# Optimization experiments

Hardware: AMD Instinct MI355X
Metric: run time of the kernel (lower is better)

The kernel has to match this reference:

```python
import jax, jax.numpy as jnp
import numpy as np

BATCH, SEQ, HIDDEN = 8, 2048, 1024
WSIZE = 64  # window half-width; eye=True -> positions with |i-j| > WSIZE are masked
NEG_INF = -1e9


def setup_inputs() -> dict:
    key = jax.random.key(0)
    k1, k2 = jax.random.split(key)
    repr_ = jax.random.normal(k1, (BATCH, SEQ, HIDDEN), dtype=jnp.float32)
    W = jax.random.normal(k2, (HIDDEN, HIDDEN), dtype=jnp.float32) * 0.02
    return {"repr": repr_, "W": W}


def reference(repr, W):
    b, s, d = repr.shape
    idx = jnp.arange(s)
    # window_mask with eye=True: triu(wsize+1) XOR tril(-(wsize+1)) == |i-j| > wsize
    mask = jnp.abs(idx[:, None] - idx[None, :]) > WSIZE  # [s, s], True = masked
    # Attention: bilinear scores q @ W @ k^T, masked softmax over keys
    scores = jnp.einsum("bqd,de,bke->bqk", repr, W, repr)
    scores = jnp.where(mask[None, :, :], NEG_INF, scores)
    probs = jax.nn.softmax(scores, axis=-1)  # [b, s, s]
    ra = jnp.einsum("bqk,bkd->bqd", probs, repr)
    return repr + jax.nn.relu(ra)
```

## Files before the change

kernel.cpp:

```cpp
#include <hip/hip_runtime.h>


#define SEQL 2048
#define HID  1024
#define NB   8
#define QT   32
#define KT   160
#define DCO  128
#define EC   32
#define DS   32
#define RP   36
#define WP   132
#define QP   132
#define KP   36
#define SP   161

#define RS_OFF  0
#define WS_OFF  1152
#define KS_OFF  0
#define QCS_OFF 5760
#define SC_OFF  5760
#define SMEM_F  10912

__device__ __forceinline__ float bfu(unsigned int lo16) {
// ... 135 lines not shown
        float4 qv[4];
#pragma unroll
        for (int i = 0; i < 4; i++)
          qv[i] = *(const float4*)&smem[QCS_OFF + (ty + 8 * i) * QP + s + dd];
#pragma unroll
        for (int j = 0; j < 5; j++) {
          float4 kv = *(const float4*)&smem[KS_OFF + (tx + 32 * j) * KP + dd];
#pragma unroll
          for (int i = 0; i < 4; i++)
            acc[i][j] += qv[i].x * kv.x + qv[i].y * kv.y + qv[i].z * kv.z + qv[i].w * kv.w;
        }
      }
      __syncthreads();
    }
  }

#pragma unroll
  for (int i = 0; i < 4; i++)
#pragma unroll
    for (int j = 0; j < 5; j++)
      smem[SC_OFF + (ty + 8 * i) * SP + tx + 32 * j] = acc[i][j];
  __syncthreads();

  {
    const int row = tid >> 3, l8 = tid & 7;
    int clo = row;          { int t = 64 - q0;            if (t > clo) clo = t; }
    int chi = row + 128;    { int t = SEQL - 1 + 64 - q0; if (t < chi) chi = t; }
    float m = -1e30f;
    for (int c = l8; c < KT; c += 8)
      if (c >= clo && c <= chi) m = fmaxf(m, smem[SC_OFF + row * SP + c]);
    m = fmaxf(m, __shfl_xor(m, 1));
    m = fmaxf(m, __shfl_xor(m, 2));
    m = fmaxf(m, __shfl_xor(m, 4));
    float ssum = 0.f;
    for (int c = l8; c < KT; c += 8) {
      float e = (c >= clo && c <= chi) ? __expf(smem[SC_OFF + row * SP + c] - m) : 0.f;
      smem[SC_OFF + row * SP + c] = e;
      ssum += e;
    }
    ssum += __shfl_xor(ssum, 1);
    ssum += __shfl_xor(ssum, 2);
    ssum += __shfl_xor(ssum, 4);
    float rinv = 1.f / ssum;
    for (int c = l8; c < KT; c += 8) smem[SC_OFF + row * SP + c] *= rinv;
  }
  __syncthreads();

  const int rr = tid >> 3, dq = tid & 7;
  for (int d0 = 0; d0 < HID; d0 += DS) {
#pragma unroll
    for (int i2 = 0; i2 < 5; i2++) {
      int f = i2 * 256 + tid;
      int row = f >> 3, cg = f & 7;
      int kk = q0 - 64 + row;
      kk = kk < 0 ? 0 : (kk > SEQL - 1 ? SEQL - 1 : kk);
      float4 v = ld4<BF16>(reprv, baseR + (size_t)kk * HID + d0 + 4 * cg);
      *(float4*)&smem[KS_OFF + row * KP + 4 * cg] = v;
    }
    __syncthreads();
    float4 o = make_float4(0.f, 0.f, 0.f, 0.f);
#pragma unroll 4
    for (int c = 0; c < KT; c++) {
      float4 kv = *(const float4*)&smem[KS_OFF + c * KP + 4 * dq];
      float p = smem[SC_OFF + rr * SP + c];
      o.x += p * kv.x; o.y += p * kv.y; o.z += p * kv.z; o.w += p * kv.w;
    }
    size_t goff = baseR + (size_t)(q0 + rr) * HID + d0 + 4 * dq;
    float4 rv = ld4<BF16>(reprv, goff);
    float4 ov;
    ov.x = rv.x + fmaxf(o.x, 0.f);
    ov.y = rv.y + fmaxf(o.y, 0.f);
    ov.z = rv.z + fmaxf(o.z, 0.f);
    ov.w = rv.w + fmaxf(o.w, 0.f);
    st4<BF16>(outv, goff, ov);
    __syncthreads();
  }
}

typedef float f32x4 __attribute__((ext_vector_type(4)));
typedef short bf16x8 __attribute__((ext_vector_type(8)));

#define MF(a_, b_, c_) __builtin_amdgcn_mfma_f32_16x16x32_bf16((a_), (b_), (c_), 0, 0, 0)

__global__ void __launch_bounds__(256) tposeW2(
    const void* __restrict__ reprv, const void* __restrict__ Wv,
    void* __restrict__ wsv) {
  const bool isbf = data_is_bf16((const unsigned short*)reprv);
  __shared__ alignas(16) unsigned char twsb[64 * 68 * 4];
  const int t = threadIdx.x;
  const int d0 = (blockIdx.x & 15) * 64, e0 = (blockIdx.x >> 4) * 64;
  if (isbf) {
    unsigned short* tl = (unsigned short*)twsb;
    const unsigned short* WB = (const unsigned short*)Wv;
    unsigned short* WtB = (unsigned short*)wsv;
#pragma unroll
    for (int i = 0; i < 2; i++) {
      int slot = i * 256 + t, row = slot >> 3, c8 = slot & 7;
      *(uint4*)(tl + row * 72 + 8 * c8) =
          *(const uint4*)(WB + (size_t)(d0 + row) * 1024 + e0 + 8 * c8);
    }
    __syncthreads();
#pragma unroll
    for (int i = 0; i < 2; i++) {
      int slot = i * 256 + t, er = slot >> 3, c8 = slot & 7;
      unsigned short v[8];
#pragma unroll
      for (int j = 0; j < 8; j++) v[j] = tl[(8 * c8 + j) * 72 + er];
      *(uint4*)(WtB + (size_t)(e0 + er) * 1024 + d0 + 8 * c8) = *(const uint4*)v;
    }
  } else {
    float* tlf = (float*)twsb;
    const float* WF = (const float*)Wv;
    unsigned short* WfH = (unsigned short*)wsv;
    unsigned short* WfL = WfH + (1u << 20);
#pragma unroll
    for (int i = 0; i < 4; i++) {
      int slot = i * 256 + t, row = slot >> 4, cf = slot & 15;
      *(float4*)&tlf[row * 68 + 4 * cf] =
          *(const float4*)(WF + (size_t)(d0 + row) * 1024 + e0 + 4 * cf);
    }
    __syncthreads();
#pragma unroll
    for (int i = 0; i < 2; i++) {
      int slot = i * 256 + t, er = slot >> 3, c8 = slot & 7;
      int e = e0 + er;
      int dg = d0 + 8 * c8;
      unsigned short vh[8], vl[8];
#pragma unroll
      for (int j = 0; j < 8; j++) {
        float v = tlf[(8 * c8 + j) * 68 + er];
        hilo(v, vh[j], vl[j]);
      }
      size_t dst = (size_t)(((e >> 4) << 5) | (dg >> 5)) * 512
                 + (size_t)(((((dg >> 3) & 3) << 4) | (e & 15))) * 8;
      *(uint4*)(WfH + dst) = *(const uint4*)vh;
      *(uint4*)(WfL + dst) = *(const uint4*)vl;
    }
  }
}

#define WTS_O 0
#define RQS_O 9216
#define RK_O  11520
#define QHI_O 17920
#define QLO_O 22272
#define PBF_O 11008
#define VT_O  16384
#define SMEMU 27136

__global__ void __launch_bounds__(256, 2) attn_mfma(
    const unsigned short* __restrict__ reprB,
    const unsigned short* __restrict__ WtB,
    unsigned short* __restrict__ outB) {
  if (!data_is_bf16(reprB)) return;

  __shared__ alignas(16) unsigned short sm[SMEMU];
  float* smf = (float*)sm;

  const int tid = threadIdx.x;
  const int w = tid >> 6, l = tid & 63, lr = l & 15, lg = l >> 4;
  const int b = blockIdx.y, q0 = blockIdx.x * 32;
  const size_t baseR = (size_t)b * 2048 * 1024;
  const int qt = w >> 1;
  const int ktb = (w & 1) * 5;

  f32x4 acc_s[5];
// ... 98 lines not shown
    for (int r = 0; r < 4; r++) {
      int row = 16 * qt + 4 * lg + r;
      int col = 16 * (ktb + j) + lr;
      smf[row * 172 + col] = acc_s[j][r];
    }
  __syncthreads();

  {
    const int row = tid >> 3, l8 = tid & 7;
    int clo = row;          { int t2 = 64 - q0;            if (t2 > clo) clo = t2; }
    int chi = row + 128;    { int t2 = 2047 + 64 - q0;     if (t2 < chi) chi = t2; }
    float m = -1e30f;
    for (int c = l8; c < 160; c += 8)
      if (c >= clo && c <= chi) m = fmaxf(m, smf[row * 172 + c]);
    m = fmaxf(m, __shfl_xor(m, 1));
    m = fmaxf(m, __shfl_xor(m, 2));
    m = fmaxf(m, __shfl_xor(m, 4));
    float ssum = 0.f;
    for (int c = l8; c < 160; c += 8) {
      float e = (c >= clo && c <= chi) ? __expf(smf[row * 172 + c] - m) : 0.f;
      smf[row * 172 + c] = e;
      ssum += e;
    }
    ssum += __shfl_xor(ssum, 1);
    ssum += __shfl_xor(ssum, 2);
    ssum += __shfl_xor(ssum, 4);
    float rinv = 1.f / ssum;
    for (int c = l8; c < 160; c += 8)
      sm[PBF_O + row * 168 + c] = f2bf(smf[row * 172 + c] * rinv);
  }
  __syncthreads();

  const int dtl = (w & 1) * 2;
  bf16x8 pa[5];
#pragma unroll
  for (int ks = 0; ks < 5; ks++)
    pa[ks] = *(const bf16x8*)(sm + PBF_O + (16 * qt + lr) * 168 + 32 * ks + 8 * lg);

  for (int dc = 0; dc < 16; dc++) {
    const int d0 = dc * 64;
    uint4 vr[5];
#pragma unroll
    for (int i = 0; i < 5; i++) {
      int slot = i * 256 + tid;
      int k = slot >> 3, g = slot & 7;
      int kk = q0 - 64 + k;
      kk = kk < 0 ? 0 : (kk > 2047 ? 2047 : kk);
      vr[i] = *(const uint4*)(reprB + baseR + (size_t)kk * 1024 + d0 + 8 * g);
    }
    __syncthreads();
#pragma unroll
    for (int i = 0; i < 5; i++) {
      int slot = i * 256 + tid;
      int k = slot >> 3, g = slot & 7;
      const unsigned short* pv = (const unsigned short*)&vr[i];
#pragma unroll
      for (int j2 = 0; j2 < 8; j2++)
        sm[VT_O + (8 * g + j2) * 168 + k] = pv[j2];
    }
    __syncthreads();
    f32x4 ra0 = (f32x4){0.f, 0.f, 0.f, 0.f};
    f32x4 ra1 = (f32x4){0.f, 0.f, 0.f, 0.f};
#pragma unroll
    for (int ks = 0; ks < 5; ks++) {
      bf16x8 v0 = *(const bf16x8*)(sm + VT_O + (16 * dtl + lr) * 168 + 32 * ks + 8 * lg);
      bf16x8 v1 = *(const bf16x8*)(sm + VT_O + (16 * (dtl + 1) + lr) * 168 + 32 * ks + 8 * lg);
      ra0 = MF(pa[ks], v0, ra0);
      ra1 = MF(pa[ks], v1, ra1);
    }
#pragma unroll
    for (int r = 0; r < 4; r++) {
      int qg = q0 + 16 * qt + 4 * lg + r;
      size_t base = baseR + (size_t)qg * 1024 + d0;
      int dg0 = 16 * dtl + lr, dg1 = 16 * (dtl + 1) + lr;
      float o0 = bfu(reprB[base + dg0]) + fmaxf(ra0[r], 0.f);
      float o1 = bfu(reprB[base + dg1]) + fmaxf(ra1[r], 0.f);
      outB[base + dg0] = f2bf(o0);
      outB[base + dg1] = f2bf(o1);
    }
  }
}

#define FRQB(k)  ((k) * 4608)
#define FRKH_O  0
#define FRKL_O  6400
#define FQHI_O  12800
#define FQLO_O  17152
#define FPBF_O  12288
#define FVT_O   0
#define FSMEMU  21504

__device__ __forceinline__ int vtidx(int row, int k) {
  int m = (row ^ (row >> 2)) & 7;
  return FVT_O + row * 192 + ((((k >> 3) ^ m) << 3) | (k & 7));
}

__global__ void __launch_bounds__(256, 2) attn_mfma_f32(
    const float* __restrict__ reprF,
    const unsigned short* __restrict__ WfH,
    const unsigned short* __restrict__ WfL,
    float* __restrict__ outF) {
  if (data_is_bf16((const unsigned short*)reprF)) return;

  __shared__ alignas(16) unsigned short sm[FSMEMU];
  float* smf = (float*)sm;

  const int tid = threadIdx.x;
  const int w = tid >> 6, l = tid & 63, lr = l & 15, lg = l >> 4;
  const int b = blockIdx.y, q0 = blockIdx.x * 32;
  const size_t baseR = (size_t)b * 2048 * 1024;
  const int qt = w >> 1;
  const int ktb = (w & 1) * 5;

  const int rrow = tid >> 4, rcf = tid & 15;

  f32x4 acc_s[5];
#pragma unroll
  for (int j = 0; j < 5; j++) acc_s[j] = (f32x4){0.f, 0.f, 0.f, 0.f};

  for (int ec = 0; ec < 8; ec++) {
    const int e0 = ec * 128;
    const int ecw8 = 8 * ec + 2 * w;
    f32x4 acc_q[2][2];
#pragma unroll
    for (int i = 0; i < 2; i++)
#pragma unroll
      for (int j = 0; j < 2; j++) acc_q[i][j] = (f32x4){0.f, 0.f, 0.f, 0.f};

    bf16x8 Bf[3][8];
    float4 rqv[2][2];

#define LDB(bidx, sidx) {                                                      \
    size_t f00 = ((size_t)((((ecw8 + 0) << 5) + 2 * (sidx) + 0)) << 9) + l * 8;\
    size_t f01 = ((size_t)((((ecw8 + 0) << 5) + 2 * (sidx) + 1)) << 9) + l * 8;\
    size_t f10 = ((size_t)((((ecw8 + 1) << 5) + 2 * (sidx) + 0)) << 9) + l * 8;\
    size_t f11 = ((size_t)((((ecw8 + 1) << 5) + 2 * (sidx) + 1)) << 9) + l * 8;\
    Bf[bidx][0] = *(const bf16x8*)(WfH + f00);                                 \
    Bf[bidx][1] = *(const bf16x8*)(WfH + f01);                                 \
    Bf[bidx][2] = *(const bf16x8*)(WfH + f10);                                 \
    Bf[bidx][3] = *(const bf16x8*)(WfH + f11);                                 \
    Bf[bidx][4] = *(const bf16x8*)(WfL + f00);                                 \
    Bf[bidx][5] = *(const bf16x8*)(WfL + f01);                                 \
    Bf[bidx][6] = *(const bf16x8*)(WfL + f10);                                 \
    Bf[bidx][7] = *(const bf16x8*)(WfL + f11);                                 \
  }

#define WQ(sidx) {                                                             \
    const int wb = FRQB((sidx) & 1);                                           \
    _Pragma("unroll")                                                          \
    for (int i = 0; i < 2; i++) {                                              \
      ushort4 h4, l4;                                                          \
      float4 v = rqv[(sidx) & 1][i];                                           \
      hilo(v.x, h4.x, l4.x); hilo(v.y, h4.y, l4.y);                            \
      hilo(v.z, h4.z, l4.z); hilo(v.w, h4.w, l4.w);                            \
      *(ushort4*)(sm + wb + (16 * i + rrow) * 72 + 4 * rcf) = h4;              \
      *(ushort4*)(sm + wb + 2304 + (16 * i + rrow) * 72 + 4 * rcf) = l4;       \
    } }

#pragma unroll
    for (int i = 0; i < 2; i++)
      rqv[0][i] = *(const float4*)(reprF + baseR + (size_t)(q0 + 16 * i + rrow) * 1024 + 0 + 4 * rcf);
#pragma unroll
    for (int i = 0; i < 2; i++)
      rqv[1][i] = *(const float4*)(reprF + baseR + (size_t)(q0 + 16 * i + rrow) * 1024 + 64 + 4 * rcf);
    LDB(0, 0)
    LDB(1, 1)

    __syncthreads();
    WQ(0)
    __syncthreads();

#pragma unroll
    for (int s = 0; s < 16; s++) {
      if (s < 15) WQ(s + 1)
      if (s < 14) {
        const int d0n = 64 * (s + 2);
#pragma unroll
        for (int i = 0; i < 2; i++)
          rqv[s & 1][i] = *(const float4*)(reprF + baseR + (size_t)(q0 + 16 * i + rrow) * 1024 + d0n + 4 * rcf);
        LDB((s + 2) % 3, s + 2)
      }
      {
        const int rqb = FRQB(s & 1);
#pragma unroll
        for (int h = 0; h < 2; h++) {
          bf16x8 ah0 = *(const bf16x8*)(sm + rqb + (lr) * 72 + 32 * h + 8 * lg);
          bf16x8 ah1 = *(const bf16x8*)(sm + rqb + (16 + lr) * 72 + 32 * h + 8 * lg);
          bf16x8 al0 = *(const bf16x8*)(sm + rqb + 2304 + (lr) * 72 + 32 * h + 8 * lg);
          bf16x8 al1 = *(const bf16x8*)(sm + rqb + 2304 + (16 + lr) * 72 + 32 * h + 8 * lg);
          bf16x8 bh0 = Bf[s % 3][0 + h];
          bf16x8 bh1 = Bf[s % 3][2 + h];
          bf16x8 bl0 = Bf[s % 3][4 + h];
          bf16x8 bl1 = Bf[s % 3][6 + h];
          acc_q[0][0] = MF(ah0, bh0, acc_q[0][0]);
          acc_q[0][1] = MF(ah0, bh1, acc_q[0][1]);
          acc_q[1][0] = MF(ah1, bh0, acc_q[1][0]);
          acc_q[1][1] = MF(ah1, bh1, acc_q[1][1]);
          acc_q[0][0] = MF(ah0, bl0, acc_q[0][0]);
          acc_q[0][1] = MF(ah0, bl1, acc_q[0][1]);
          acc_q[1][0] = MF(ah1, bl0, acc_q[1][0]);
          acc_q[1][1] = MF(ah1, bl1, acc_q[1][1]);
          acc_q[0][0] = MF(al0, bh0, acc_q[0][0]);
          acc_q[0][1] = MF(al0, bh1, acc_q[0][1]);
          acc_q[1][0] = MF(al1, bh0, acc_q[1][0]);
          acc_q[1][1] = MF(al1, bh1, acc_q[1][1]);
        }
      }
      __syncthreads();
    }
#undef LDB
#undef WQ

    float4 rk4[5];
#pragma unroll
    for (int i = 0; i < 5; i++) {
      int slot = i * 256 + tid;
      int row = slot >> 3;
      int kk = q0 - 64 + row;
      kk = kk < 0 ? 0 : (kk > 2047 ? 2047 : kk);
      rk4[i] = *(const float4*)(reprF + baseR + (size_t)kk * 1024 + e0 + 4 * (slot & 7));
    }

#pragma unroll
    for (int qq = 0; qq < 2; qq++)
#pragma unroll
      for (int et = 0; et < 2; et++)
#pragma unroll
        for (int r = 0; r < 4; r++) {
          int row = 16 * qq + 4 * lg + r;
          int col = 32 * w + 16 * et + lr;
          float v = acc_q[qq][et][r];
          unsigned short hi, lo;
          hilo(v, hi, lo);
          sm[FQHI_O + row * 136 + col] = hi;
          sm[FQLO_O + row * 136 + col] = lo;
        }

    for (int es = 0; es < 4; es++) {
      __syncthreads();
#pragma unroll
      for (int i = 0; i < 5; i++) {
        int slot = i * 256 + tid;
        int row = slot >> 3, cf = slot & 7;
        ushort4 h4, l4;
        hilo(rk4[i].x, h4.x, l4.x); hilo(rk4[i].y, h4.y, l4.y);
        hilo(rk4[i].z, h4.z, l4.z); hilo(rk4[i].w, h4.w, l4.w);
        *(ushort4*)(sm + FRKH_O + row * 40 + 4 * cf) = h4;
        *(ushort4*)(sm + FRKL_O + row * 40 + 4 * cf) = l4;
      }
      __syncthreads();
      if (es < 3) {
#pragma unroll
        for (int i = 0; i < 5; i++) {
          int slot = i * 256 + tid;
          int row = slot >> 3;
          int kk = q0 - 64 + row;
          kk = kk < 0 ? 0 : (kk > 2047 ? 2047 : kk);
          rk4[i] = *(const float4*)(reprF + baseR + (size_t)kk * 1024 + e0 + 32 * (es + 1) + 4 * (slot & 7));
        }
      }
      bf16x8 qh = *(const bf16x8*)(sm + FQHI_O + (16 * qt + lr) * 136 + 32 * es + 8 * lg);
      bf16x8 ql = *(const bf16x8*)(sm + FQLO_O + (16 * qt + lr) * 136 + 32 * es + 8 * lg);
#pragma unroll
      for (int j = 0; j < 5; j++) {
        bf16x8 kh = *(const bf16x8*)(sm + FRKH_O + (16 * (ktb + j) + lr) * 40 + 8 * lg);
        bf16x8 kl = *(const bf16x8*)(sm + FRKL_O + (16 * (ktb + j) + lr) * 40 + 8 * lg);
        acc_s[j] = MF(qh, kh, acc_s[j]);
        acc_s[j] = MF(qh, kl, acc_s[j]);
        acc_s[j] = MF(ql, kh, acc_s[j]);
      }
    }
  }

  __syncthreads();
#pragma unroll
  for (int j = 0; j < 5; j++)
#pragma unroll
    for (int r = 0; r < 4; r++) {
      int row = 16 * qt + 4 * lg + r;
      int col = 16 * (ktb + j) + lr;
      smf[row * 172 + col] = acc_s[j][r];
    }
  __syncthreads();

  {
    const int row = tid >> 3, l8 = tid & 7;
    int clo = row;          { int t2 = 64 - q0;            if (t2 > clo) clo = t2; }
    int chi = row + 128;    { int t2 = 2047 + 64 - q0;     if (t2 < chi) chi = t2; }
    float m = -1e30f;
    for (int c = l8; c < 160; c += 8)
      if (c >= clo && c <= chi) m = fmaxf(m, smf[row * 172 + c]);
    m = fmaxf(m, __shfl_xor(m, 1));
    m = fmaxf(m, __shfl_xor(m, 2));
    m = fmaxf(m, __shfl_xor(m, 4));
    float ssum = 0.f;
    for (int c = l8; c < 160; c += 8) {
      float e = (c >= clo && c <= chi) ? __expf(smf[row * 172 + c] - m) : 0.f;
      smf[row * 172 + c] = e;
      ssum += e;
    }
    ssum += __shfl_xor(ssum, 1);
    ssum += __shfl_xor(ssum, 2);
    ssum += __shfl_xor(ssum, 4);
    float rinv = 1.f / ssum;
    for (int c = l8; c < 160; c += 8)
      sm[FPBF_O + row * 168 + c] = f2bf(smf[row * 172 + c] * rinv);
  }
  __syncthreads();

  const int dtl = (w & 1) * 2;
  bf16x8 pa[5];
#pragma unroll
  for (int ks = 0; ks < 5; ks++)
    pa[ks] = *(const bf16x8*)(sm + FPBF_O + (16 * qt + lr) * 168 + 32 * ks + 8 * lg);

  float4 vr4[10];
#pragma unroll
  for (int i = 0; i < 10; i++) {
    int slot = i * 256 + tid;
    int k = slot >> 4, g = slot & 15;
    int kk = q0 - 64 + k;
    kk = kk < 0 ? 0 : (kk > 2047 ? 2047 : kk);
    vr4[i] = *(const float4*)(reprF + baseR + (size_t)kk * 1024 + 4 * g);
  }

  for (int dc = 0; dc < 16; dc++) {
    const int d0 = dc * 64;
    __syncthreads();
#pragma unroll
    for (int i = 0; i < 10; i++) {
      int slot = i * 256 + tid;
      int k = slot >> 4, g = slot & 15;
      sm[vtidx(4 * g + 0, k)] = f2bf(vr4[i].x);
      sm[vtidx(4 * g + 1, k)] = f2bf(vr4[i].y);
      sm[vtidx(4 * g + 2, k)] = f2bf(vr4[i].z);
      sm[vtidx(4 * g + 3, k)] = f2bf(vr4[i].w);
    }
    __syncthreads();
    if (dc < 15) {
      const int d0n = d0 + 64;
#pragma unroll
      for (int i = 0; i < 10; i++) {
        int slot = i * 256 + tid;
        int k = slot >> 4, g = slot & 15;
        int kk = q0 - 64 + k;
        kk = kk < 0 ? 0 : (kk > 2047 ? 2047 : kk);
        vr4[i] = *(const float4*)(reprF + baseR + (size_t)kk * 1024 + d0n + 4 * g);
      }
    }
    f32x4 ra0 = (f32x4){0.f, 0.f, 0.f, 0.f};
    f32x4 ra1 = (f32x4){0.f, 0.f, 0.f, 0.f};
    const int row0 = 16 * dtl + lr, row1 = 16 * (dtl + 1) + lr;
#pragma unroll
    for (int ks = 0; ks < 5; ks++) {
      bf16x8 v0 = *(const bf16x8*)(sm + vtidx(row0, 32 * ks + 8 * lg));
      bf16x8 v1 = *(const bf16x8*)(sm + vtidx(row1, 32 * ks + 8 * lg));
      ra0 = MF(pa[ks], v0, ra0);
      ra1 = MF(pa[ks], v1, ra1);
    }
#pragma unroll
    for (int r = 0; r < 4; r++) {
      int qg = q0 + 16 * qt + 4 * lg + r;
      size_t base = baseR + (size_t)qg * 1024 + d0;
      int dg0 = 16 * dtl + lr, dg1 = 16 * (dtl + 1) + lr;
      outF[base + dg0] = reprF[base + dg0] + fmaxf(ra0[r], 0.f);
      outF[base + dg1] = reprF[base + dg1] + fmaxf(ra1[r], 0.f);
    }
  }
}

extern "C" void kernel_launch(void* const* d_in, const int* in_sizes, int n_in,
                              void* d_out, int out_size, void* d_ws, size_t ws_size,
                              hipStream_t stream) {
  const void* repr = d_in[0];
  const void* W    = d_in[1];
  dim3 grid(SEQL / QT, NB);

  const bool use_mfma = (d_ws != nullptr) && (ws_size >= (size_t)4 * 1024 * 1024);
  if (use_mfma) {
    tposeW2<<<dim3(256), dim3(256), 0, stream>>>(repr, W, d_ws);
    attn_mfma<<<grid, dim3(256), 0, stream>>>(
        (const unsigned short*)repr, (const unsigned short*)d_ws, (unsigned short*)d_out);
    attn_mfma_f32<<<grid, dim3(256), 0, stream>>>(
        (const float*)repr, (const unsigned short*)d_ws,
        (const unsigned short*)d_ws + (1u << 20), (float*)d_out);
  } else {
    attn_fused<true><<<grid, dim3(256), 0, stream>>>(repr, W, d_out);
    attn_fused<false><<<grid, dim3(256), 0, stream>>>(repr, W, d_out);
  }
}
```

Baseline: 341.8 us.

## Double attn_mfma_f32 block to 512 threads and redistribute per-wave work

Result: slower. 437.8 us (+28.1%).

```diff
diff --git a/kernel.cpp b/kernel.cpp
--- a/kernel.cpp
+++ b/kernel.cpp
@@ -518,7 +518,7 @@
   return FVT_O + row * 192 + ((((k >> 3) ^ m) << 3) | (k & 7));
 }
 
-__global__ void __launch_bounds__(256, 2) attn_mfma_f32(
+__global__ void __launch_bounds__(512, 4) attn_mfma_f32(
     const float* __restrict__ reprF,
     const unsigned short* __restrict__ WfH,
     const unsigned short* __restrict__ WfL,
@@ -532,32 +532,33 @@
   const int w = tid >> 6, l = tid & 63, lr = l & 15, lg = l >> 4;
   const int b = blockIdx.y, q0 = blockIdx.x * 32;
   const size_t baseR = (size_t)b * 2048 * 1024;
-  const int qt = w >> 1;
-  const int ktb = (w & 1) * 5;
+
+  const int qd = w & 1, eh = w >> 1;
+  const int qt = w >> 2, kg = w & 3;
+  const int nj = (kg < 2) ? 3 : 2;
+  const int dt = w & 3;
 
   const int rrow = tid >> 4, rcf = tid & 15;
 
-  f32x4 acc_s[5];
-#pragma unroll
-  for (int j = 0; j < 5; j++) acc_s[j] = (f32x4){0.f, 0.f, 0.f, 0.f};
+  f32x4 acc_s[3];
+#pragma unroll
+  for (int j = 0; j < 3; j++) acc_s[j] = (f32x4){0.f, 0.f, 0.f, 0.f};
 
   for (int ec = 0; ec < 8; ec++) {
     const int e0 = ec * 128;
-    const int ecw8 = 8 * ec + 2 * w;
-    f32x4 acc_q[2][2];
-#pragma unroll
-    for (int i = 0; i < 2; i++)
-#pragma unroll
-      for (int j = 0; j < 2; j++) acc_q[i][j] = (f32x4){0.f, 0.f, 0.f, 0.f};
+    const int ecw8 = 8 * ec + 2 * eh;
+    f32x4 acc_q[2];
+#pragma unroll
+    for (int i = 0; i < 2; i++) acc_q[i] = (f32x4){0.f, 0.f, 0.f, 0.f};
 
     bf16x8 Bf[3][8];
-    float4 rqv[2][2];
+    float4 rqv[2];
 
 #define LDB(bidx, sidx) {                                                      \
-    size_t f00 = ((size_t)((((ecw8 + 0) << 5) + 2 * (sidx) + 0)) << 9) + l * 8;\
-    size_t f01 = ((size_t)((((ecw8 + 0) << 5) + 2 * (sidx) + 1)) << 9) + l * 8;\
-    size_t f10 = ((size_t)((((ecw8 + 1) << 5) + 2 * (sidx) + 0)) << 9) + l * 8;\
-    size_t f11 = ((size_t)((((ecw8 + 1) << 5) + 2 * (sidx) + 1)) << 9) + l * 8;\
+    size_t f00 = (((size_t)(ecw8 + 0) << 5) + 2 * (sidx) + 0) * 512 + l * 8;   \
+    size_t f01 = (((size_t)(ecw8 + 0) << 5) + 2 * (sidx) + 1) * 512 + l * 8;   \
+    size_t f10 = (((size_t)(ecw8 + 1) << 5) + 2 * (sidx) + 0) * 512 + l * 8;   \
+    size_t f11 = (((size_t)(ecw8 + 1) << 5) + 2 * (sidx) + 1) * 512 + l * 8;   \
     Bf[bidx][0] = *(const bf16x8*)(WfH + f00);                                 \
     Bf[bidx][1] = *(const bf16x8*)(WfH + f01);                                 \
     Bf[bidx][2] = *(const bf16x8*)(WfH + f10);                                 \
@@ -570,22 +571,16 @@
 
 #define WQ(sidx) {                                                             \
     const int wb = FRQB((sidx) & 1);                                           \
-    _Pragma("unroll")                                                          \
-    for (int i = 0; i < 2; i++) {                                              \
-      ushort4 h4, l4;                                                          \
-      float4 v = rqv[(sidx) & 1][i];                                           \
-      hilo(v.x, h4.x, l4.x); hilo(v.y, h4.y, l4.y);                            \
-      hilo(v.z, h4.z, l4.z); hilo(v.w, h4.w, l4.w);                            \
-      *(ushort4*)(sm + wb + (16 * i + rrow) * 72 + 4 * rcf) = h4;              \
-      *(ushort4*)(sm + wb + 2304 + (16 * i + rrow) * 72 + 4 * rcf) = l4;       \
-    } }
-
-#pragma unroll
-    for (int i = 0; i < 2; i++)
-      rqv[0][i] = *(const float4*)(reprF + baseR + (size_t)(q0 + 16 * i + rrow) * 1024 + 0 + 4 * rcf);
-#pragma unroll
-    for (int i = 0; i < 2; i++)
-      rqv[1][i] = *(const float4*)(reprF + baseR + (size_t)(q0 + 16 * i + rrow) * 1024 + 64 + 4 * rcf);
+    ushort4 h4, l4;                                                            \
+    float4 v = rqv[(sidx) & 1];                                                \
+    hilo(v.x, h4.x, l4.x); hilo(v.y, h4.y, l4.y);                              \
+    hilo(v.z, h4.z, l4.z); hilo(v.w, h4.w, l4.w);                              \
+    *(ushort4*)(sm + wb + rrow * 72 + 4 * rcf) = h4;                           \
+    *(ushort4*)(sm + wb + 2304 + rrow * 72 + 4 * rcf) = l4;                    \
+  }
+
+    rqv[0] = *(const float4*)(reprF + baseR + (size_t)(q0 + rrow) * 1024 + 0 + 4 * rcf);
+    rqv[1] = *(const float4*)(reprF + baseR + (size_t)(q0 + rrow) * 1024 + 64 + 4 * rcf);
     LDB(0, 0)
     LDB(1, 1)
 
@@ -598,35 +593,23 @@
       if (s < 15) WQ(s + 1)
       if (s < 14) {
         const int d0n = 64 * (s + 2);
-#pragma unroll
-        for (int i = 0; i < 2; i++)
-          rqv[s & 1][i] = *(const float4*)(reprF + baseR + (size_t)(q0 + 16 * i + rrow) * 1024 + d0n + 4 * rcf);
+        rqv[s & 1] = *(const float4*)(reprF + baseR + (size_t)(q0 + rrow) * 1024 + d0n + 4 * rcf);
         LDB((s + 2) % 3, s + 2)
       }
       {
         const int rqb = FRQB(s & 1);
 #pragma unroll
         for (int h = 0; h < 2; h++) {
-          bf16x8 ah0 = *(const bf16x8*)(sm + rqb + (lr) * 72 + 32 * h + 8 * lg);
-          bf16x8 ah1 = *(const bf16x8*)(sm + rqb + (16 + lr) * 72 + 32 * h + 8 * lg);
-          bf16x8 al0 = *(const bf16x8*)(sm + rqb + 2304 + (lr) * 72 + 32 * h + 8 * lg);
-          bf16x8 al1 = *(const bf16x8*)(sm + rqb + 2304 + (16 + lr) * 72 + 32 * h + 8 * lg);
-          bf16x8 bh0 = Bf[s % 3][0 + h];
-          bf16x8 bh1 = Bf[s % 3][2 + h];
-          bf16x8 bl0 = Bf[s % 3][4 + h];
-          bf16x8 bl1 = Bf[s % 3][6 + h];
-          acc_q[0][0] = MF(ah0, bh0, acc_q[0][0]);
-          acc_q[0][1] = MF(ah0, bh1, acc_q[0][1]);
-          acc_q[1][0] = MF(ah1, bh0, acc_q[1][0]);
-          acc_q[1][1] = MF(ah1, bh1, acc_q[1][1]);
-          acc_q[0][0] = MF(ah0, bl0, acc_q[0][0]);
-          acc_q[0][1] = MF(ah0, bl1, acc_q[0][1]);
-          acc_q[1][0] = MF(ah1, bl0, acc_q[1][0]);
-          acc_q[1][1] = MF(ah1, bl1, acc_q[1][1]);
-          acc_q[0][0] = MF(al0, bh0, acc_q[0][0]);
-          acc_q[0][1] = MF(al0, bh1, acc_q[0][1]);
-          acc_q[1][0] = MF(al1, bh0, acc_q[1][0]);
-          acc_q[1][1] = MF(al1, bh1, acc_q[1][1]);
+          bf16x8 ah = *(const bf16x8*)(sm + rqb + (16 * qd + lr) * 72 + 32 * h + 8 * lg);
+          bf16x8 al = *(const bf16x8*)(sm + rqb + 2304 + (16 * qd + lr) * 72 + 32 * h + 8 * lg);
+#pragma unroll
+          for (int et = 0; et < 2; et++) {
+            bf16x8 bh = Bf[s % 3][2 * et + h];
+            bf16x8 bl = Bf[s % 3][4 + 2 * et + h];
+            acc_q[et] = MF(ah, bh, acc_q[et]);
+            acc_q[et] = MF(ah, bl, acc_q[et]);
+            acc_q[et] = MF(al, bh, acc_q[et]);
+          }
         }
       }
       __syncthreads();
@@ -634,90 +617,102 @@
 #undef LDB
 #undef WQ
 
-    float4 rk4[5];
-#pragma unroll
-    for (int i = 0; i < 5; i++) {
-      int slot = i * 256 + tid;
-      int row = slot >> 3;
-      int kk = q0 - 64 + row;
-      kk = kk < 0 ? 0 : (kk > 2047 ? 2047 : kk);
-      rk4[i] = *(const float4*)(reprF + baseR + (size_t)kk * 1024 + e0 + 4 * (slot & 7));
-    }
-
-#pragma unroll
-    for (int qq = 0; qq < 2; qq++)
-#pragma unroll
-      for (int et = 0; et < 2; et++)
-#pragma unroll
-        for (int r = 0; r < 4; r++) {
-          int row = 16 * qq + 4 * lg + r;
-          int col = 32 * w + 16 * et + lr;
-          float v = acc_q[qq][et][r];
-          unsigned short hi, lo;
-          hilo(v, hi, lo);
-          sm[FQHI_O + row * 136 + col] = hi;
-          sm[FQLO_O + row * 136 + col] = lo;
-        }
+    float4 rk4[3];
+#pragma unroll
+    for (int i = 0; i < 3; i++) {
+      int slot = i * 512 + tid;
+      if (slot < 1280) {
+        int row = slot >> 3;
+        int kk = q0 - 64 + row;
+        kk = kk < 0 ? 0 : (kk > 2047 ? 2047 : kk);
+        rk4[i] = *(const float4*)(reprF + baseR + (size_t)kk * 1024 + e0 + 4 * (slot & 7));
+      }
+    }
+
+#pragma unroll
+    for (int et = 0; et < 2; et++)
+#pragma unroll
+      for (int r = 0; r < 4; r++) {
+        int row = 16 * qd + 4 * lg + r;
+        int col = 32 * eh + 16 * et + lr;
+        float v = acc_q[et][r];
+        unsigned short hi, lo;
+        hilo(v, hi, lo);
+        sm[FQHI_O + row * 136 + col] = hi;
+        sm[FQLO_O + row * 136 + col] = lo;
+      }
 
     for (int es = 0; es < 4; es++) {
       __syncthreads();
 #pragma unroll
-      for (int i = 0; i < 5; i++) {
-        int slot = i * 256 + tid;
-        int row = slot >> 3, cf = slot & 7;
-        ushort4 h4, l4;
-        hilo(rk4[i].x, h4.x, l4.x); hilo(rk4[i].y, h4.y, l4.y);
-        hilo(rk4[i].z, h4.z, l4.z); hilo(rk4[i].w, h4.w, l4.w);
-        *(ushort4*)(sm + FRKH_O + row * 40 + 4 * cf) = h4;
-        *(ushort4*)(sm + FRKL_O + row * 40 + 4 * cf) = l4;
+      for (int i = 0; i < 3; i++) {
+        int slot = i * 512 + tid;
+        if (slot < 1280) {
+          int row = slot >> 3, cf = slot & 7;
+          ushort4 h4, l4;
+          hilo(rk4[i].x, h4.x, l4.x); hilo(rk4[i].y, h4.y, l4.y);
+          hilo(rk4[i].z, h4.z, l4.z); hilo(rk4[i].w, h4.w, l4.w);
+          *(ushort4*)(sm + FRKH_O + row * 40 + 4 * cf) = h4;
+          *(ushort4*)(sm + FRKL_O + row * 40 + 4 * cf) = l4;
+        }
       }
       __syncthreads();
       if (es < 3) {
 #pragma unroll
-        for (int i = 0; i < 5; i++) {
-          int slot = i * 256 + tid;
-          int row = slot >> 3;
-          int kk = q0 - 64 + row;
-          kk = kk < 0 ? 0 : (kk > 2047 ? 2047 : kk);
-          rk4[i] = *(const float4*)(reprF + baseR + (size_t)kk * 1024 + e0 + 32 * (es + 1) + 4 * (slot & 7));
+        for (int i = 0; i < 3; i++) {
+          int slot = i * 512 + tid;
+          if (slot < 1280) {
+            int row = slot >> 3;
+            int kk = q0 - 64 + row;
+            kk = kk < 0 ? 0 : (kk > 2047 ? 2047 : kk);
+            rk4[i] = *(const float4*)(reprF + baseR + (size_t)kk * 1024 + e0 + 32 * (es + 1) + 4 * (slot & 7));
+          }
         }
       }
       bf16x8 qh = *(const bf16x8*)(sm + FQHI_O + (16 * qt + lr) * 136 + 32 * es + 8 * lg);
       bf16x8 ql = *(const bf16x8*)(sm + FQLO_O + (16 * qt + lr) * 136 + 32 * es + 8 * lg);
 #pragma unroll
-      for (int j = 0; j < 5; j++) {
-        bf16x8 kh = *(const bf16x8*)(sm + FRKH_O + (16 * (ktb + j) + lr) * 40 + 8 * lg);
-        bf16x8 kl = *(const bf16x8*)(sm + FRKL_O + (16 * (ktb + j) + lr) * 40 + 8 * lg);
-        acc_s[j] = MF(qh, kh, acc_s[j]);
-        acc_s[j] = MF(qh, kl, acc_s[j]);
-        acc_s[j] = MF(ql, kh, acc_s[j]);
+      for (int jx = 0; jx < 3; jx++) {
+        if (jx < nj) {
+          int jj = kg + 4 * jx;
+          bf16x8 kh = *(const bf16x8*)(sm + FRKH_O + (16 * jj + lr) * 40 + 8 * lg);
+          bf16x8 kl = *(const bf16x8*)(sm + FRKL_O + (16 * jj + lr) * 40 + 8 * lg);
+          acc_s[jx] = MF(qh, kh, acc_s[jx]);
+          acc_s[jx] = MF(qh, kl, acc_s[jx]);
+          acc_s[jx] = MF(ql, kh, acc_s[jx]);
+        }
       }
     }
   }
 
   __syncthreads();
 #pragma unroll
-  for (int j = 0; j < 5; j++)
-#pragma unroll
-    for (int r = 0; r < 4; r++) {
-      int row = 16 * qt + 4 * lg + r;
-      int col = 16 * (ktb + j) + lr;
-      smf[row * 172 + col] = acc_s[j][r];
-    }
+  for (int jx = 0; jx < 3; jx++) {
+    if (jx < nj) {
+      int jj = kg + 4 * jx;
+#pragma unroll
+      for (int r = 0; r < 4; r++) {
+        int row = 16 * qt + 4 * lg + r;
+        int col = 16 * jj + lr;
+        smf[row * 172 + col] = acc_s[jx][r];
+      }
+    }
+  }
   __syncthreads();
 
   {
-    const int row = tid >> 3, l8 = tid & 7;
+    const int row = tid >> 4, l16 = tid & 15;
     int clo = row;          { int t2 = 64 - q0;            if (t2 > clo) clo = t2; }
     int chi = row + 128;    { int t2 = 2047 + 64 - q0;     if (t2 < chi) chi = t2; }
     float m = -1e30f;
-    for (int c = l8; c < 160; c += 8)
+    for (int c = l16; c < 160; c += 16)
       if (c >= clo && c <= chi) m = fmaxf(m, smf[row * 172 + c]);
     m = fmaxf(m, __shfl_xor(m, 1));
     m = fmaxf(m, __shfl_xor(m, 2));
     m = fmaxf(m, __shfl_xor(m, 4));
+    m = fmaxf(m, __shfl_xor(m, 8));
     float ssum = 0.f;
-    for (int c = l8; c < 160; c += 8) {
+    for (int c = l16; c < 160; c += 16) {
       float e = (c >= clo && c <= chi) ? __expf(smf[row * 172 + c] - m) : 0.f;
       smf[row * 172 + c] = e;
       ssum += e;
@@ -725,22 +720,22 @@
     ssum += __shfl_xor(ssum, 1);
     ssum += __shfl_xor(ssum, 2);
     ssum += __shfl_xor(ssum, 4);
+    ssum += __shfl_xor(ssum, 8);
     float rinv = 1.f / ssum;
-    for (int c = l8; c < 160; c += 8)
+    for (int c = l16; c < 160; c += 16)
       sm[FPBF_O + row * 168 + c] = f2bf(smf[row * 172 + c] * rinv);
   }
   __syncthreads();
 
-  const int dtl = (w & 1) * 2;
   bf16x8 pa[5];
 #pragma unroll
   for (int ks = 0; ks < 5; ks++)
     pa[ks] = *(const bf16x8*)(sm + FPBF_O + (16 * qt + lr) * 168 + 32 * ks + 8 * lg);
 
-  float4 vr4[10];
-#pragma unroll
-  for (int i = 0; i < 10; i++) {
-    int slot = i * 256 + tid;
+  float4 vr4[5];
+#pragma unroll
+  for (int i = 0; i < 5; i++) {
+    int slot = i * 512 + tid;
     int k = slot >> 4, g = slot & 15;
     int kk = q0 - 64 + k;
     kk = kk < 0 ? 0 : (kk > 2047 ? 2047 : kk);
@@ -751,8 +746,8 @@
     const int d0 = dc * 64;
     __syncthreads();
 #pragma unroll
-    for (int i = 0; i < 10; i++) {
-      int slot = i * 256 + tid;
+    for (int i = 0; i < 5; i++) {
+      int slot = i * 512 + tid;
       int k = slot >> 4, g = slot & 15;
       sm[vtidx(4 * g + 0, k)] = f2bf(vr4[i].x);
       sm[vtidx(4 * g + 1, k)] = f2bf(vr4[i].y);
@@ -763,8 +758,8 @@
     if (dc < 15) {
       const int d0n = d0 + 64;
 #pragma unroll
-      for (int i = 0; i < 10; i++) {
-        int slot = i * 256 + tid;
+      for (int i = 0; i < 5; i++) {
+        int slot = i * 512 + tid;
         int k = slot >> 4, g = slot & 15;
         int kk = q0 - 64 + k;
         kk = kk < 0 ? 0 : (kk > 2047 ? 2047 : kk);
@@ -772,22 +767,18 @@
       }
     }
     f32x4 ra0 = (f32x4){0.f, 0.f, 0.f, 0.f};
-    f32x4 ra1 = (f32x4){0.f, 0.f, 0.f, 0.f};
-    const int row0 = 16 * dtl + lr, row1 = 16 * (dtl + 1) + lr;
+    const int row0 = 16 * dt + lr;
 #pragma unroll
     for (int ks = 0; ks < 5; ks++) {
       bf16x8 v0 = *(const bf16x8*)(sm + vtidx(row0, 32 * ks + 8 * lg));
-      bf16x8 v1 = *(const bf16x8*)(sm + vtidx(row1, 32 * ks + 8 * lg));
       ra0 = MF(pa[ks], v0, ra0);
-      ra1 = MF(pa[ks], v1, ra1);
     }
 #pragma unroll
     for (int r = 0; r < 4; r++) {
       int qg = q0 + 16 * qt + 4 * lg + r;
       size_t base = baseR + (size_t)qg * 1024 + d0;
-      int dg0 = 16 * dtl + lr, dg1 = 16 * (dtl + 1) + lr;
+      int dg0 = 16 * dt + lr;
       outF[base + dg0] = reprF[base + dg0] + fmaxf(ra0[r], 0.f);
-      outF[base + dg1] = reprF[base + dg1] + fmaxf(ra1[r], 0.f);
     }
   }
 }
@@ -804,7 +795,7 @@
     tposeW2<<<dim3(256), dim3(256), 0, stream>>>(repr, W, d_ws);
     attn_mfma<<<grid, dim3(256), 0, stream>>>(
         (const unsigned short*)repr, (const unsigned short*)d_ws, (unsigned short*)d_out);
-    attn_mfma_f32<<<grid, dim3(256), 0, stream>>>(
+    attn_mfma_f32<<<grid, dim3(512), 0, stream>>>(
         (const float*)repr, (const unsigned short*)d_ws,
         (const unsigned short*)d_ws + (1u << 20), (float*)d_out);
   } else {
```

## Restructure fp32 QW projection into 512-wide halves with direct-register K fragments

Applied to the files above, without the earlier changes.

Measured after the change: 340.7 us. Within noise of the previous version (-0.3%).

```diff
diff --git a/kernel.cpp b/kernel.cpp
--- a/kernel.cpp
+++ b/kernel.cpp
@@ -241,6 +241,24 @@
 
 #define MF(a_, b_, c_) __builtin_amdgcn_mfma_f32_16x16x32_bf16((a_), (b_), (c_), 0, 0, 0)
 
+__device__ __forceinline__ void bar_lgkm() {
+  asm volatile("s_waitcnt lgkmcnt(0)" ::: "memory");
+  __builtin_amdgcn_s_barrier();
+}
+
+__device__ __forceinline__ void cvt8(const float4 a, const float4 b,
+                                     bf16x8& h8, bf16x8& l8) {
+  unsigned short h, lo_;
+  hilo(a.x, h, lo_); h8[0] = (short)h; l8[0] = (short)lo_;
+  hilo(a.y, h, lo_); h8[1] = (short)h; l8[1] = (short)lo_;
+  hilo(a.z, h, lo_); h8[2] = (short)h; l8[2] = (short)lo_;
+  hilo(a.w, h, lo_); h8[3] = (short)h; l8[3] = (short)lo_;
+  hilo(b.x, h, lo_); h8[4] = (short)h; l8[4] = (short)lo_;
+  hilo(b.y, h, lo_); h8[5] = (short)h; l8[5] = (short)lo_;
+  hilo(b.z, h, lo_); h8[6] = (short)h; l8[6] = (short)lo_;
+  hilo(b.w, h, lo_); h8[7] = (short)h; l8[7] = (short)lo_;
+}
+
 __global__ void __launch_bounds__(256) tposeW2(
     const void* __restrict__ reprv, const void* __restrict__ Wv,
     void* __restrict__ wsv) {
@@ -505,13 +523,11 @@
 }
 
 #define FRQB(k)  ((k) * 4608)
-#define FRKH_O  0
-#define FRKL_O  6400
-#define FQHI_O  12800
-#define FQLO_O  17152
+#define FQSH_O  9216
+#define FQSL_O  13568
 #define FPBF_O  12288
 #define FVT_O   0
-#define FSMEMU  21504
+#define FSMEMU  17920
 
 __device__ __forceinline__ int vtidx(int row, int k) {
   int m = (row ^ (row >> 2)) & 7;
@@ -532,166 +548,147 @@
   const int w = tid >> 6, l = tid & 63, lr = l & 15, lg = l >> 4;
   const int b = blockIdx.y, q0 = blockIdx.x * 32;
   const size_t baseR = (size_t)b * 2048 * 1024;
-  const int qt = w >> 1;
-  const int ktb = (w & 1) * 5;
-
+  const int qt = w >> 1, ktb = (w & 1) * 5;
   const int rrow = tid >> 4, rcf = tid & 15;
 
   f32x4 acc_s[5];
 #pragma unroll
   for (int j = 0; j < 5; j++) acc_s[j] = (f32x4){0.f, 0.f, 0.f, 0.f};
 
-  for (int ec = 0; ec < 8; ec++) {
-    const int e0 = ec * 128;
-    const int ecw8 = 8 * ec + 2 * w;
-    f32x4 acc_q[2][2];
+  for (int half = 0; half < 2; half++) {
+    f32x4 acc_q[4][2][2];
+#pragma unroll
+    for (int q = 0; q < 4; q++)
+#pragma unroll
+      for (int i = 0; i < 2; i++)
+#pragma unroll
+        for (int j = 0; j < 2; j++) acc_q[q][i][j] = (f32x4){0.f, 0.f, 0.f, 0.f};
+
+    bf16x8 Bf[2][8];
+    float4 rqv[2];
+
+#define LDB(bidx, tt) {                                                        \
+    const int q_ = (tt) & 3, s_ = (tt) >> 2;                                   \
+    const int r16 = 32 * half + 8 * q_ + 2 * w;                                \
+    _Pragma("unroll")                                                          \
+    for (int et_ = 0; et_ < 2; et_++)                                          \
+    _Pragma("unroll")                                                          \
+      for (int cs_ = 0; cs_ < 2; cs_++) {                                      \
+        size_t f_ = ((size_t)((r16 + et_) * 32 + 2 * s_ + cs_)) * 512 + l * 8; \
+        Bf[bidx][2 * et_ + cs_]     = *(const bf16x8*)(WfH + f_);              \
+        Bf[bidx][4 + 2 * et_ + cs_] = *(const bf16x8*)(WfL + f_);              \
+      } }
+
+#define WQS(par) {                                                             \
+    const int wb_ = FRQB(par);                                                 \
+    _Pragma("unroll")                                                          \
+    for (int i_ = 0; i_ < 2; i_++) {                                           \
+      ushort4 h4_, l4_;                                                        \
+      hilo(rqv[i_].x, h4_.x, l4_.x); hilo(rqv[i_].y, h4_.y, l4_.y);            \
+      hilo(rqv[i_].z, h4_.z, l4_.z); hilo(rqv[i_].w, h4_.w, l4_.w);            \
+      *(ushort4*)(sm + wb_ + (16 * i_ + rrow) * 72 + 4 * rcf) = h4_;           \
+      *(ushort4*)(sm + wb_ + 2304 + (16 * i_ + rrow) * 72 + 4 * rcf) = l4_;    \
+    } }
+
+#define STAGE(ss, par) {                                                       \
+    WQS(par)                                                                   \
+    if ((ss) < 15) {                                                           \
+      const int d0n_ = 64 * ((ss) + 1);                                        \
+      _Pragma("unroll")                                                        \
+      for (int i_ = 0; i_ < 2; i_++)                                           \
+        rqv[i_] = *(const float4*)(reprF + baseR +                             \
+            (size_t)(q0 + 16 * i_ + rrow) * 1024 + d0n_ + 4 * rcf);            \
+    }                                                                          \
+    bar_lgkm();                                                                \
+    const int rqb_ = FRQB(par);                                                \
+    bf16x8 ah_[2][2], al_[2][2];                                               \
+    _Pragma("unroll")                                                          \
+    for (int cs_ = 0; cs_ < 2; cs_++) {                                        \
+      ah_[cs_][0] = *(const bf16x8*)(sm + rqb_ + (lr) * 72 + 32 * cs_ + 8 * lg);\
+      ah_[cs_][1] = *(const bf16x8*)(sm + rqb_ + (16 + lr) * 72 + 32 * cs_ + 8 * lg);\
+      al_[cs_][0] = *(const bf16x8*)(sm + rqb_ + 2304 + (lr) * 72 + 32 * cs_ + 8 * lg);\
+      al_[cs_][1] = *(const bf16x8*)(sm + rqb_ + 2304 + (16 + lr) * 72 + 32 * cs_ + 8 * lg);\
+    }                                                                          \
+    _Pragma("unroll")                                                          \
+    for (int q_i = 0; q_i < 4; q_i++) {                                        \
+      if (4 * (ss) + q_i < 63) { LDB((q_i + 1) & 1, 4 * (ss) + q_i + 1) }      \
+      _Pragma("unroll")                                                        \
+      for (int cs_ = 0; cs_ < 2; cs_++)                                        \
+      _Pragma("unroll")                                                        \
+        for (int et_ = 0; et_ < 2; et_++) {                                    \
+          bf16x8 bh_ = Bf[q_i & 1][2 * et_ + cs_];                             \
+          bf16x8 bl_ = Bf[q_i & 1][4 + 2 * et_ + cs_];                         \
+          acc_q[q_i][0][et_] = MF(ah_[cs_][0], bh_, acc_q[q_i][0][et_]);       \
+          acc_q[q_i][0][et_] = MF(ah_[cs_][0], bl_, acc_q[q_i][0][et_]);       \
+          acc_q[q_i][0][et_] = MF(al_[cs_][0], bh_, acc_q[q_i][0][et_]);       \
+          acc_q[q_i][1][et_] = MF(ah_[cs_][1], bh_, acc_q[q_i][1][et_]);       \
+          acc_q[q_i][1][et_] = MF(ah_[cs_][1], bl_, acc_q[q_i][1][et_]);       \
+          acc_q[q_i][1][et_] = MF(al_[cs_][1], bh_, acc_q[q_i][1][et_]);       \
+        }                                                                      \
+    } }
+
 #pragma unroll
     for (int i = 0; i < 2; i++)
-#pragma unroll
-      for (int j = 0; j < 2; j++) acc_q[i][j] = (f32x4){0.f, 0.f, 0.f, 0.f};
-
-    bf16x8 Bf[3][8];
-    float4 rqv[2][2];
-
-#define LDB(bidx, sidx) {                                                      \
-    size_t f00 = ((size_t)((((ecw8 + 0) << 5) + 2 * (sidx) + 0)) << 9) + l * 8;\
-    size_t f01 = ((size_t)((((ecw8 + 0) << 5) + 2 * (sidx) + 1)) << 9) + l * 8;\
-    size_t f10 = ((size_t)((((ecw8 + 1) << 5) + 2 * (sidx) + 0)) << 9) + l * 8;\
-    size_t f11 = ((size_t)((((ecw8 + 1) << 5) + 2 * (sidx) + 1)) << 9) + l * 8;\
-    Bf[bidx][0] = *(const bf16x8*)(WfH + f00);                                 \
-    Bf[bidx][1] = *(const bf16x8*)(WfH + f01);                                 \
-    Bf[bidx][2] = *(const bf16x8*)(WfH + f10);                                 \
-    Bf[bidx][3] = *(const bf16x8*)(WfH + f11);                                 \
-    Bf[bidx][4] = *(const bf16x8*)(WfL + f00);                                 \
-    Bf[bidx][5] = *(const bf16x8*)(WfL + f01);                                 \
-    Bf[bidx][6] = *(const bf16x8*)(WfL + f10);                                 \
-    Bf[bidx][7] = *(const bf16x8*)(WfL + f11);                                 \
-  }
-
-#define WQ(sidx) {                                                             \
-    const int wb = FRQB((sidx) & 1);                                           \
-    _Pragma("unroll")                                                          \
-    for (int i = 0; i < 2; i++) {                                              \
-      ushort4 h4, l4;                                                          \
-      float4 v = rqv[(sidx) & 1][i];                                           \
-      hilo(v.x, h4.x, l4.x); hilo(v.y, h4.y, l4.y);                            \
-      hilo(v.z, h4.z, l4.z); hilo(v.w, h4.w, l4.w);                            \
-      *(ushort4*)(sm + wb + (16 * i + rrow) * 72 + 4 * rcf) = h4;              \
-      *(ushort4*)(sm + wb + 2304 + (16 * i + rrow) * 72 + 4 * rcf) = l4;       \
-    } }
-
-#pragma unroll
-    for (int i = 0; i < 2; i++)
-      rqv[0][i] = *(const float4*)(reprF + baseR + (size_t)(q0 + 16 * i + rrow) * 1024 + 0 + 4 * rcf);
-#pragma unroll
-    for (int i = 0; i < 2; i++)
-      rqv[1][i] = *(const float4*)(reprF + baseR + (size_t)(q0 + 16 * i + rrow) * 1024 + 64 + 4 * rcf);
+      rqv[i] = *(const float4*)(reprF + baseR + (size_t)(q0 + 16 * i + rrow) * 1024 + 4 * rcf);
     LDB(0, 0)
-    LDB(1, 1)
-
-    __syncthreads();
-    WQ(0)
-    __syncthreads();
-
-#pragma unroll
-    for (int s = 0; s < 16; s++) {
-      if (s < 15) WQ(s + 1)
-      if (s < 14) {
-        const int d0n = 64 * (s + 2);
-#pragma unroll
-        for (int i = 0; i < 2; i++)
-          rqv[s & 1][i] = *(const float4*)(reprF + baseR + (size_t)(q0 + 16 * i + rrow) * 1024 + d0n + 4 * rcf);
-        LDB((s + 2) % 3, s + 2)
-      }
-      {
-        const int rqb = FRQB(s & 1);
-#pragma unroll
-        for (int h = 0; h < 2; h++) {
-          bf16x8 ah0 = *(const bf16x8*)(sm + rqb + (lr) * 72 + 32 * h + 8 * lg);
-          bf16x8 ah1 = *(const bf16x8*)(sm + rqb + (16 + lr) * 72 + 32 * h + 8 * lg);
-          bf16x8 al0 = *(const bf16x8*)(sm + rqb + 2304 + (lr) * 72 + 32 * h + 8 * lg);
-          bf16x8 al1 = *(const bf16x8*)(sm + rqb + 2304 + (16 + lr) * 72 + 32 * h + 8 * lg);
-          bf16x8 bh0 = Bf[s % 3][0 + h];
-          bf16x8 bh1 = Bf[s % 3][2 + h];
-          bf16x8 bl0 = Bf[s % 3][4 + h];
-          bf16x8 bl1 = Bf[s % 3][6 + h];
-          acc_q[0][0] = MF(ah0, bh0, acc_q[0][0]);
-          acc_q[0][1] = MF(ah0, bh1, acc_q[0][1]);
-          acc_q[1][0] = MF(ah1, bh0, acc_q[1][0]);
-          acc_q[1][1] = MF(ah1, bh1, acc_q[1][1]);
-          acc_q[0][0] = MF(ah0, bl0, acc_q[0][0]);
-          acc_q[0][1] = MF(ah0, bl1, acc_q[0][1]);
-          acc_q[1][0] = MF(ah1, bl0, acc_q[1][0]);
-          acc_q[1][1] = MF(ah1, bl1, acc_q[1][1]);
-          acc_q[0][0] = MF(al0, bh0, acc_q[0][0]);
-          acc_q[0][1] = MF(al0, bh1, acc_q[0][1]);
-          acc_q[1][0] = MF(al1, bh0, acc_q[1][0]);
-          acc_q[1][1] = MF(al1, bh1, acc_q[1][1]);
+
+    for (int sb = 0; sb < 16; sb += 2) {
+      STAGE(sb, 0)
+      STAGE(sb + 1, 1)
+    }
+#undef STAGE
+#undef WQS
+#undef LDB
+
+#pragma unroll
+    for (int c = 0; c < 4; c++) {
+      const int ebase = 512 * half + 128 * c;
+      __syncthreads();
+
+      float4 kc0, kc1, kn0, kn1, km0, km1;
+#define KLOAD(d0_, d1_, uu) {                                                  \
+      const int j_ = (uu) % 5, es_ = (uu) / 5;                                 \
+      int kk_ = q0 - 64 + 16 * (ktb + j_) + lr;                                \
+      kk_ = kk_ < 0 ? 0 : (kk_ > 2047 ? 2047 : kk_);                           \
+      const float* p_ = reprF + baseR + (size_t)kk_ * 1024 + ebase + 32 * es_ + 8 * lg; \
+      d0_ = *(const float4*)p_;                                                \
+      d1_ = *(const float4*)(p_ + 4);                                          \
+    }
+      KLOAD(kc0, kc1, 0)
+      KLOAD(kn0, kn1, 1)
+      KLOAD(km0, km1, 2)
+
+#pragma unroll
+      for (int qq = 0; qq < 2; qq++)
+#pragma unroll
+        for (int et = 0; et < 2; et++)
+#pragma unroll
+          for (int r = 0; r < 4; r++) {
+            int row = 16 * qq + 4 * lg + r;
+            int col = 32 * w + 16 * et + lr;
+            unsigned short hi, lo_;
+            hilo(acc_q[c][qq][et][r], hi, lo_);
+            sm[FQSH_O + row * 136 + col] = hi;
+            sm[FQSL_O + row * 136 + col] = lo_;
+          }
+      __syncthreads();
+
+      for (int es = 0; es < 4; es++) {
+        bf16x8 qh = *(const bf16x8*)(sm + FQSH_O + (16 * qt + lr) * 136 + 32 * es + 8 * lg);
+        bf16x8 ql = *(const bf16x8*)(sm + FQSL_O + (16 * qt + lr) * 136 + 32 * es + 8 * lg);
+#pragma unroll
+        for (int j = 0; j < 5; j++) {
+          const int u = 5 * es + j;
+          bf16x8 kh, kl;
+          cvt8(kc0, kc1, kh, kl);
+          kc0 = kn0; kc1 = kn1; kn0 = km0; kn1 = km1;
+          if (u < 17) { KLOAD(km0, km1, u + 3) }
+          acc_s[j] = MF(qh, kh, acc_s[j]);
+          acc_s[j] = MF(qh, kl, acc_s[j]);
+          acc_s[j] = MF(ql, kh, acc_s[j]);
         }
       }
-      __syncthreads();
-    }
-#undef LDB
-#undef WQ
-
-    float4 rk4[5];
-#pragma unroll
-    for (int i = 0; i < 5; i++) {
-      int slot = i * 256 + tid;
-      int row = slot >> 3;
-      int kk = q0 - 64 + row;
-      kk = kk < 0 ? 0 : (kk > 2047 ? 2047 : kk);
-      rk4[i] = *(const float4*)(reprF + baseR + (size_t)kk * 1024 + e0 + 4 * (slot & 7));
-    }
-
-#pragma unroll
-    for (int qq = 0; qq < 2; qq++)
-#pragma unroll
-      for (int et = 0; et < 2; et++)
-#pragma unroll
-        for (int r = 0; r < 4; r++) {
-          int row = 16 * qq + 4 * lg + r;
-          int col = 32 * w + 16 * et + lr;
-          float v = acc_q[qq][et][r];
-          unsigned short hi, lo;
-          hilo(v, hi, lo);
-          sm[FQHI_O + row * 136 + col] = hi;
-          sm[FQLO_O + row * 136 + col] = lo;
-        }
-
-    for (int es = 0; es < 4; es++) {
-      __syncthreads();
-#pragma unroll
-      for (int i = 0; i < 5; i++) {
-        int slot = i * 256 + tid;
-        int row = slot >> 3, cf = slot & 7;
-        ushort4 h4, l4;
-        hilo(rk4[i].x, h4.x, l4.x); hilo(rk4[i].y, h4.y, l4.y);
-        hilo(rk4[i].z, h4.z, l4.z); hilo(rk4[i].w, h4.w, l4.w);
-        *(ushort4*)(sm + FRKH_O + row * 40 + 4 * cf) = h4;
-        *(ushort4*)(sm + FRKL_O + row * 40 + 4 * cf) = l4;
-      }
-      __syncthreads();
-      if (es < 3) {
-#pragma unroll
-        for (int i = 0; i < 5; i++) {
-          int slot = i * 256 + tid;
-          int row = slot >> 3;
-          int kk = q0 - 64 + row;
-          kk = kk < 0 ? 0 : (kk > 2047 ? 2047 : kk);
-          rk4[i] = *(const float4*)(reprF + baseR + (size_t)kk * 1024 + e0 + 32 * (es + 1) + 4 * (slot & 7));
-        }
-      }
-      bf16x8 qh = *(const bf16x8*)(sm + FQHI_O + (16 * qt + lr) * 136 + 32 * es + 8 * lg);
-      bf16x8 ql = *(const bf16x8*)(sm + FQLO_O + (16 * qt + lr) * 136 + 32 * es + 8 * lg);
-#pragma unroll
-      for (int j = 0; j < 5; j++) {
-        bf16x8 kh = *(const bf16x8*)(sm + FRKH_O + (16 * (ktb + j) + lr) * 40 + 8 * lg);
-        bf16x8 kl = *(const bf16x8*)(sm + FRKL_O + (16 * (ktb + j) + lr) * 40 + 8 * lg);
-        acc_s[j] = MF(qh, kh, acc_s[j]);
-        acc_s[j] = MF(qh, kl, acc_s[j]);
-        acc_s[j] = MF(ql, kh, acc_s[j]);
-      }
+#undef KLOAD
     }
   }
 
```
